# Kernel tuning notes

Hardware: AMD Instinct MI355X
Metric: run time of the kernel (lower is better)

Reference implementation:

```python
import jax, jax.numpy as jnp
import numpy as np

B, S, R, D_NODE, D_PAIR, N_HEAD, C = 1, 128, 256, 256, 128, 8, 32
EPS = 1e-5


def layer_norm(x, g, b):
    mu = jnp.mean(x, axis=-1, keepdims=True)
    var = jnp.mean(jnp.square(x - mu), axis=-1, keepdims=True)
    return (x - mu) * jax.lax.rsqrt(var + EPS) * g + b


def self_attention(x, qkv_w, qkv_b, gate_w, gate_b, o_w, o_b, bias=None):
    # x: [B, n1, n2, d]; attends over n2. heads: n_head x c, n_head*c == d.
    b_, n1, n2, d = x.shape
    qkv = x @ qkv_w.T + qkv_b                      # [B, n1, n2, 3*h*c]
    q, k, v = jnp.split(qkv, 3, axis=-1)
    split_heads = lambda t: t.reshape(b_, n1, n2, N_HEAD, C).transpose(0, 1, 3, 2, 4)  # [B,n1,h,n2,c]
    q = split_heads(q) * (C ** -0.5)
    k = split_heads(k)
    v = split_heads(v)
    logits = jnp.einsum('bshqc,bshkc->bshqk', q, k)  # [B, n1, h, n2, n2]
    if bias is not None:
        logits = logits + bias[:, None]              # bias: [B, h, n2, n2]
    w = jax.nn.softmax(logits, axis=-1)
    o = jnp.einsum('bshqk,bshkc->bshqc', w, v)
    o = o.transpose(0, 1, 3, 2, 4).reshape(b_, n1, n2, N_HEAD * C)
    gate = jax.nn.sigmoid(x @ gate_w.T + gate_b)
    o = o * gate
    out = o @ o_w.T
    if o_b is not None:
        out = out + o_b
    return out


def setup_inputs() -> dict:
    key = jax.random.key(0)
    ks = jax.random.split(key, 12)
    rn = lambda k, sh, sc=1.0: jax.random.normal(k, sh, dtype=jnp.float32) * sc
    return {
        'node': rn(ks[0], (B, S, R, D_NODE)),
        'pair': rn(ks[1], (B, R, R, D_PAIR)),
        'ln_mr_g': jnp.ones((D_NODE,), jnp.float32), 'ln_mr_b': jnp.zeros((D_NODE,), jnp.float32),
        'ln_z_g': jnp.ones((D_PAIR,), jnp.float32), 'ln_z_b': jnp.zeros((D_PAIR,), jnp.float32),
        'b_weights': rn(ks[2], (N_HEAD, D_PAIR), D_PAIR ** -0.5),
        'row_qkv_w': rn(ks[3], (3 * N_HEAD * C, D_NODE), D_NODE ** -0.5),
        'row_qkv_b': jnp.zeros((3 * N_HEAD * C,), jnp.float32),
        'row_gate_w': rn(ks[4], (N_HEAD * C, D_NODE), D_NODE ** -0.5),
        'row_gate_b': jnp.ones((N_HEAD * C,), jnp.float32),
        'row_o_w': rn(ks[5], (D_NODE, N_HEAD * C), D_NODE ** -0.5),
        'out_bias': jnp.zeros((D_NODE,), jnp.float32),
        'ln_mc_g': jnp.ones((D_NODE,), jnp.float32), 'ln_mc_b': jnp.zeros((D_NODE,), jnp.float32),
        'col_qkv_w': rn(ks[6], (3 * N_HEAD * C, D_NODE), D_NODE ** -0.5),
        'col_qkv_b': jnp.zeros((3 * N_HEAD * C,), jnp.float32),
        'col_gate_w': rn(ks[7], (N_HEAD * C, D_NODE), D_NODE ** -0.5),
        'col_gate_b': jnp.ones((N_HEAD * C,), jnp.float32),
        'col_o_w': rn(ks[8], (D_NODE, N_HEAD * C), D_NODE ** -0.5),
        'col_o_b': jnp.zeros((D_NODE,), jnp.float32),
        'ln_t_g': jnp.ones((D_NODE,), jnp.float32), 'ln_t_b': jnp.zeros((D_NODE,), jnp.float32),
        't_w1': rn(ks[9], (4 * D_NODE, D_NODE), D_NODE ** -0.5),
        't_b1': jnp.zeros((4 * D_NODE,), jnp.float32),
        't_w2': rn(ks[10], (D_NODE, 4 * D_NODE), (4 * D_NODE) ** -0.5),
        't_b2': jnp.zeros((D_NODE,), jnp.float32),
    }


def reference(node, pair, ln_mr_g, ln_mr_b, ln_z_g, ln_z_b, b_weights,
              row_qkv_w, row_qkv_b, row_gate_w, row_gate_b, row_o_w, out_bias,
              ln_mc_g, ln_mc_b, col_qkv_w, col_qkv_b, col_gate_w, col_gate_b, col_o_w, col_o_b,
              ln_t_g, ln_t_b, t_w1, t_b1, t_w2, t_b2):
    # --- MSARowAttentionWithPairBias ---
    M = layer_norm(node, ln_mr_g, ln_mr_b)                 # [B,S,R,D]
    Z = layer_norm(pair, ln_z_g, ln_z_b)                   # [B,R,R,Dp]
    b = jnp.einsum('bqkd,hd->bhqk', Z, b_weights)          # pair bias [B,h,R,R]
    M = self_attention(M, row_qkv_w, row_qkv_b, row_gate_w, row_gate_b, row_o_w, None, bias=b)
    # bias_dropout_add with ones dropout mask (inference): residual + (x + bias)
    node = node + M + out_bias
    # --- MSAColumnAttention ---
    Mt = node.transpose(0, 2, 1, 3)                        # [B,R,S,D], attend over S
    Mt = layer_norm(Mt, ln_mc_g, ln_mc_b)
    Mt = self_attention(Mt, col_qkv_w, col_qkv_b, col_gate_w, col_gate_b, col_o_w, col_o_b)
    node = node + Mt.transpose(0, 2, 1, 3)
    # --- MSATransition (n=4) ---
    x = layer_norm(node, ln_t_g, ln_t_b)
    x = jax.nn.relu(x @ t_w1.T + t_b1) @ t_w2.T + t_b2
    return node + x
```

## Files before the change

kernel.cpp:

```cpp
#include <hip/hip_runtime.h>
#include <hip/hip_bf16.h>

#define EPS 1e-5f

typedef __hip_bfloat16 bf16;
typedef __attribute__((ext_vector_type(8))) short short8v;
typedef __attribute__((ext_vector_type(4))) short short4v;
typedef __attribute__((ext_vector_type(4))) float f32x4;

__device__ inline f32x4 mfma16bf(short4v a, short4v b, f32x4 c) {
#if __has_builtin(__builtin_amdgcn_mfma_f32_16x16x16bf16_1k)
  return __builtin_amdgcn_mfma_f32_16x16x16bf16_1k(a, b, c, 0, 0, 0);
#else
  short8v a8 = {a[0], a[1], a[2], a[3], 0, 0, 0, 0};
  short8v b8 = {b[0], b[1], b[2], b[3], 0, 0, 0, 0};
  return __builtin_amdgcn_mfma_f32_16x16x32_bf16(a8, b8, c, 0, 0, 0);
#endif
}

__device__ inline void load_lds16(const void* g, void* l) {
  __builtin_amdgcn_global_load_lds(
      (const __attribute__((address_space(1))) void*)g,
      (__attribute__((address_space(3))) void*)l, 16, 0, 0);
}

__device__ inline unsigned pack_bf16x2(float a, float b) {
  union { bf16 h[2]; unsigned u; } cv;
  cv.h[0] = __float2bfloat16(a);
  cv.h[1] = __float2bfloat16(b);
  return cv.u;
}

__global__ __launch_bounds__(256) void cvt_bf16_kernel(
    const float* __restrict__ in, bf16* __restrict__ out, int n4) {
  int i = blockIdx.x * 256 + threadIdx.x;
  if (i >= n4) return;
  float4 v = reinterpret_cast<const float4*>(in)[i];
  union { ushort4 u; bf16 h[4]; } cv;
  cv.h[0] = __float2bfloat16(v.x);
  cv.h[1] = __float2bfloat16(v.y);
  cv.h[2] = __float2bfloat16(v.z);
  cv.h[3] = __float2bfloat16(v.w);
  reinterpret_cast<ushort4*>(out)[i] = cv.u;
}

__global__ __launch_bounds__(64) void ln256_bf_kernel(
    const float* __restrict__ in, bf16* __restrict__ out,
    const float* __restrict__ g, const float* __restrict__ b) {
  int row = blockIdx.x;
  int lane = threadIdx.x;
  float4 x = reinterpret_cast<const float4*>(in + (size_t)row * 256)[lane];
  float s = x.x + x.y + x.z + x.w;
  float sq = x.x * x.x + x.y * x.y + x.z * x.z + x.w * x.w;
#pragma unroll
  for (int off = 32; off >= 1; off >>= 1) {
    s += __shfl_xor(s, off);
    sq += __shfl_xor(sq, off);
  }
  float mean = s * (1.0f / 256.0f);
  float inv = rsqrtf(sq * (1.0f / 256.0f) - mean * mean + EPS);
  float4 gv = reinterpret_cast<const float4*>(g)[lane];
  float4 bv = reinterpret_cast<const float4*>(b)[lane];
  union { ushort4 u; bf16 h[4]; } cv;
  cv.h[0] = __float2bfloat16((x.x - mean) * inv * gv.x + bv.x);
  cv.h[1] = __float2bfloat16((x.y - mean) * inv * gv.y + bv.y);
  cv.h[2] = __float2bfloat16((x.z - mean) * inv * gv.z + bv.z);
  cv.h[3] = __float2bfloat16((x.w - mean) * inv * gv.w + bv.w);
  reinterpret_cast<ushort4*>(out + (size_t)row * 256)[lane] = cv.u;
}

__global__ __launch_bounds__(64) void pair_bias_kernel(
    const float* __restrict__ pair, const float* __restrict__ g,
    const float* __restrict__ b, const float* __restrict__ bw,
    bf16* __restrict__ bT) {
  int idx = blockIdx.x;
  int q = idx >> 8;
  int k = idx & 255;
  int lane = threadIdx.x;
  float2 z = reinterpret_cast<const float2*>(pair + (size_t)idx * 128)[lane];
  float s = z.x + z.y;
  float sq = z.x * z.x + z.y * z.y;
#pragma unroll
  for (int off = 32; off >= 1; off >>= 1) {
    s += __shfl_xor(s, off);
    sq += __shfl_xor(sq, off);
  }
  float mean = s * (1.0f / 128.0f);
  float inv = rsqrtf(sq * (1.0f / 128.0f) - mean * mean + EPS);
  float2 gv = reinterpret_cast<const float2*>(g)[lane];
  float2 bv = reinterpret_cast<const float2*>(b)[lane];
  float z0 = (z.x - mean) * inv * gv.x + bv.x;
  float z1 = (z.y - mean) * inv * gv.y + bv.y;
#pragma unroll
  for (int h = 0; h < 8; ++h) {
    float2 w = reinterpret_cast<const float2*>(bw + h * 128)[lane];
    float p = z0 * w.x + z1 * w.y;
#pragma unroll
    for (int off = 32; off >= 1; off >>= 1) p += __shfl_xor(p, off);
    if (lane == 0) bT[((size_t)h * 256 + q) * 256 + k] = __float2bfloat16(p);
  }
}

template <int EPI, int AMAP, int OMAP>
__global__ __launch_bounds__(256) void gemm_mfma_kernel(
    const bf16* __restrict__ A, const bf16* __restrict__ W,
    const float* __restrict__ bias, const float* __restrict__ aux, void* out,
    int N, int K, int nbn) {
  __shared__ __align__(16) short As[2][128 * 32];
  __shared__ __align__(16) short Bs[2][128 * 32];
  int nwg = gridDim.x;
  int qch = nwg >> 3;
  int flat = blockIdx.x;
  int wg = (flat & 7) * qch + (flat >> 3);
  int bm = wg / nbn, bn = wg % nbn;
  int tid = threadIdx.x;
  int w = tid >> 6, lane = tid & 63;
  int wr = w >> 1, wc = w & 1;
  int c0 = w * 64 + lane;
  int srow = c0 >> 2, skq = c0 & 3;
  const short* Aptr = (const short*)A;
  const short* Wbase = (const short*)(W + (size_t)(bn * 128) * K);
  f32x4 acc[4][4] = {};
  int lrow = lane & 15, kq = lane >> 4;

  auto arow = [&](int r) -> size_t {
    return AMAP ? ((size_t)r * 256 + bm) : ((size_t)(bm * 128 + r));
  };
  auto stage = [&](int buf, int k0) {
    load_lds16(Aptr + arow(srow) * K + k0 + skq * 8, &As[buf][c0 * 8]);
    load_lds16(Aptr + arow(srow + 64) * K + k0 + skq * 8,
               &As[buf][(256 + c0) * 8]);
    load_lds16(Wbase + (size_t)srow * K + k0 + skq * 8, &Bs[buf][c0 * 8]);
    load_lds16(Wbase + (size_t)(srow + 64) * K + k0 + skq * 8,
               &Bs[buf][(256 + c0) * 8]);
  };

  stage(0, 0);
  __syncthreads();
  int nk = K >> 5;
  for (int t = 0; t < nk; ++t) {
    int cur = t & 1;
    if (t + 1 < nk) stage(cur ^ 1, (t + 1) << 5);
    short8v af[4], bfv[4];
#pragma unroll
    for (int i = 0; i < 4; ++i)
      af[i] = *reinterpret_cast<const short8v*>(
          &As[cur][(wr * 64 + i * 16 + lrow) * 32 + kq * 8]);
#pragma unroll
    for (int j = 0; j < 4; ++j)
      bfv[j] = *reinterpret_cast<const short8v*>(
          &Bs[cur][(wc * 64 + j * 16 + lrow) * 32 + kq * 8]);
#pragma unroll
    for (int i = 0; i < 4; ++i)
#pragma unroll
      for (int j = 0; j < 4; ++j)
        acc[i][j] = __builtin_amdgcn_mfma_f32_16x16x32_bf16(af[i], bfv[j],
                                                            acc[i][j], 0, 0, 0);
    __syncthreads();
  }

  float* outF = (float*)out;
  bf16* outB = (bf16*)out;
  int r4 = (lane >> 4) * 4;
#pragma unroll
  for (int j = 0; j < 4; ++j) {
    int c = bn * 128 + wc * 64 + j * 16 + lrow;
    float bv = bias ? bias[c] : 0.0f;
#pragma unroll
    for (int i = 0; i < 4; ++i) {
      int lr0 = wr * 64 + i * 16 + r4;
#pragma unroll
      for (int reg = 0; reg < 4; ++reg) {
        int lr = lr0 + reg;
        size_t off = OMAP ? (((size_t)lr * 256 + bm) * N + c)
                          : ((size_t)(bm * 128 + lr) * N + c);
        float v = acc[i][j][reg] + bv;
        if (EPI == 0) {
          outB[off] = __float2bfloat16(v);
        } else if (EPI == 2) {
          outF[off] = v + aux[off];
        } else {
          outB[off] = __float2bfloat16(fmaxf(v, 0.0f));
        }
      }
    }
  }
}

template <bool ROWMODE>
__global__ __launch_bounds__(512) void attn_mfma_kernel(
    const bf16* __restrict__ qkv, const bf16* __restrict__ bT,
    bf16* __restrict__ o) {
  constexpr int KVLEN = ROWMODE ? 256 : 128;
  constexpr int QT = ROWMODE ? 2 : 1;
  constexpr int KOUT = KVLEN / 64;
  constexpr int STRIDE = 1024;
  constexpr int NT = 512;
  __shared__ __align__(16) short K_lds[KVLEN * 32];
  __shared__ __align__(16) short Vt_lds[32 * KVLEN];

  int b = blockIdx.x;
  int idx = b >> 3, h = b & 7;
  const short* qb = (const short*)qkv + (size_t)idx * (KVLEN * 1024);
  const bf16* qbh = (const bf16*)qb;
  bf16* ob = o + (size_t)idx * (KVLEN * 256);
  int tid = threadIdx.x;
  int w = tid >> 6, lane = tid & 63;
  int l15 = lane & 15, l4 = lane >> 4;

#pragma unroll
  for (int rnd = 0; rnd < (KVLEN * 4) / NT; ++rnd) {
    int c = rnd * NT + tid;
    int row = c >> 2;
    int kq = (c & 3) ^ ((row >> 1) & 3);
    load_lds16(qb + (size_t)row * STRIDE + 256 + h * 32 + kq * 8,
               &K_lds[c * 8]);
  }
  {
    int tt = tid;
    if (KVLEN * 2 == NT || tt < KVLEN * 2) {
      int kp = tt >> 2;
      int cc = (tt & 3) * 8;
      short8v va = *reinterpret_cast<const short8v*>(
          qb + (size_t)(2 * kp) * STRIDE + 512 + h * 32 + cc);
      short8v vb = *reinterpret_cast<const short8v*>(
          qb + (size_t)(2 * kp + 1) * STRIDE + 512 + h * 32 + cc);
      int k = 2 * kp;
      int u = k >> 3;
      int klo = k & 7;
#pragma unroll
      for (int e = 0; e < 8; ++e) {
        int cI = cc + e;
        int up = u ^ (cI & 7);
        unsigned pk = (unsigned)(unsigned short)va[e] |
                      ((unsigned)(unsigned short)vb[e] << 16);
        *reinterpret_cast<unsigned*>(&Vt_lds[cI * KVLEN + up * 8 + klo]) = pk;
      }
    }
  }
  __syncthreads();

  int q0 = w * QT * 16;
  short8v qf[QT];
#pragma unroll
  for (int j = 0; j < QT; ++j)
    qf[j] = *reinterpret_cast<const short8v*>(
        qb + (size_t)(q0 + j * 16 + l15) * STRIDE + h * 32 + l4 * 8);

  float lrun[QT];
#pragma unroll
  for (int j = 0; j < QT; ++j) lrun[j] = 0.0f;
  f32x4 acc_o[QT][2] = {};

  const float SC = 0.17677669529663687f;
  const float L2E = 1.4426950408889634f;
  const f32x4 zf = {0.f, 0.f, 0.f, 0.f};

#pragma unroll 1
  for (int kt = 0; kt < KOUT; ++kt) {
    ushort4 bb[QT][4];
    if (ROWMODE) {
#pragma unroll
      for (int j = 0; j < QT; ++j) {
        const bf16* bq = bT + (size_t)h * 65536 +
                         (size_t)(q0 + j * 16 + l15) * 256 + kt * 64 + l4 * 4;
#pragma unroll
        for (int i = 0; i < 4; ++i)
          bb[j][i] = *reinterpret_cast<const ushort4*>(bq + i * 16);
      }
    }
    short8v kf[4];
#pragma unroll
    for (int i = 0; i < 4; ++i) {
      int krow = kt * 64 + i * 16 + l15;
      kf[i] = *reinterpret_cast<const short8v*>(
          &K_lds[krow * 32 + ((l4 ^ ((krow >> 1) & 3)) * 8)]);
    }
    short4v vfa[4][2];
#pragma unroll
    for (int ks4 = 0; ks4 < 4; ++ks4)
#pragma unroll
      for (int ct = 0; ct < 2; ++ct) {
        int cI = ct * 16 + l15;
        int u = kt * 8 + ks4 * 2 + (l4 >> 1);
        vfa[ks4][ct] = *reinterpret_cast<const short4v*>(
            &Vt_lds[cI * KVLEN + (u ^ (cI & 7)) * 8 + (l4 & 1) * 4]);
      }

#pragma unroll
    for (int j = 0; j < QT; ++j) {
      f32x4 accs[4];
#pragma unroll
      for (int i = 0; i < 4; ++i)
        accs[i] =
            __builtin_amdgcn_mfma_f32_16x16x32_bf16(kf[i], qf[j], zf, 0, 0, 0);
      float sum = 0.0f;
#pragma unroll
      for (int i = 0; i < 4; ++i) {
        if (ROWMODE) {
          union { ushort4 u; bf16 h4[4]; } bu;
          bu.u = bb[j][i];
#pragma unroll
          for (int r = 0; r < 4; ++r)
            accs[i][r] = accs[i][r] * SC + __bfloat162float(bu.h4[r]);
        } else {
#pragma unroll
          for (int r = 0; r < 4; ++r) accs[i][r] *= SC;
        }
#pragma unroll
        for (int r = 0; r < 4; ++r) {
          float p = exp2f(accs[i][r] * L2E);
          accs[i][r] = p;
          sum += p;
        }
      }
      sum += __shfl_xor(sum, 16);
      sum += __shfl_xor(sum, 32);
      lrun[j] += sum;
#pragma unroll
      for (int ks4 = 0; ks4 < 4; ++ks4) {
        union { unsigned u2[2]; short4v s; } pb;
        pb.u2[0] = pack_bf16x2(accs[ks4][0], accs[ks4][1]);
        pb.u2[1] = pack_bf16x2(accs[ks4][2], accs[ks4][3]);
#pragma unroll
        for (int ct = 0; ct < 2; ++ct)
          acc_o[j][ct] = mfma16bf(vfa[ks4][ct], pb.s, acc_o[j][ct]);
      }
    }
  }

#pragma unroll
  for (int j = 0; j < QT; ++j) {
    float inv = 1.0f / lrun[j];
    int row = q0 + j * 16 + l15;
    const bf16* grow = qbh + (size_t)row * STRIDE + 768 + h * 32;
    bf16* orow = ob + (size_t)row * 256 + h * 32;
#pragma unroll
    for (int ct = 0; ct < 2; ++ct) {
      int cc = ct * 16 + l4 * 4;
      ushort4 gv = *reinterpret_cast<const ushort4*>(grow + cc);
      union { ushort4 u; bf16 h4[4]; } gu, ou;
      gu.u = gv;
#pragma unroll
      for (int r = 0; r < 4; ++r) {
        float gt = __bfloat162float(gu.h4[r]);
        float sg = 1.0f / (1.0f + __expf(-gt));
        ou.h4[r] = __float2bfloat16(acc_o[j][ct][r] * inv * sg);
      }
      *reinterpret_cast<ushort4*>(orow + cc) = ou.u;
    }
  }
}

extern "C" void kernel_launch(void* const* d_in, const int* in_sizes, int n_in,
                              void* d_out, int out_size, void* d_ws,
                              size_t ws_size, hipStream_t stream) {
  (void)in_sizes; (void)n_in; (void)out_size; (void)ws_size;
  const float* node      = (const float*)d_in[0];
  const float* pair      = (const float*)d_in[1];
  const float* ln_mr_g   = (const float*)d_in[2];
  const float* ln_mr_b   = (const float*)d_in[3];
  const float* ln_z_g    = (const float*)d_in[4];
  const float* ln_z_b    = (const float*)d_in[5];
  const float* b_weights = (const float*)d_in[6];
  const float* row_qkv_w = (const float*)d_in[7];
  const float* row_qkv_b = (const float*)d_in[8];
  const float* row_gate_w= (const float*)d_in[9];
  const float* row_gate_b= (const float*)d_in[10];
  const float* row_o_w   = (const float*)d_in[11];
  const float* out_bias  = (const float*)d_in[12];
  const float* ln_mc_g   = (const float*)d_in[13];
  const float* ln_mc_b   = (const float*)d_in[14];
  const float* col_qkv_w = (const float*)d_in[15];
  const float* col_qkv_b = (const float*)d_in[16];
  const float* col_gate_w= (const float*)d_in[17];
  const float* col_gate_b= (const float*)d_in[18];
  const float* col_o_w   = (const float*)d_in[19];
  const float* col_o_b   = (const float*)d_in[20];
  const float* ln_t_g    = (const float*)d_in[21];
  const float* ln_t_b    = (const float*)d_in[22];
  const float* t_w1      = (const float*)d_in[23];
  const float* t_b1      = (const float*)d_in[24];
  const float* t_w2      = (const float*)d_in[25];
  const float* t_b2      = (const float*)d_in[26];
  float* out = (float*)d_out;

  const size_t NR = 32768;
  char* p = (char*)d_ws;
  float* buf_node = (float*)p; p += NR * 256 * 4;
  char*  qkv_region = p;       p += NR * 1024 * 2;
  bf16* buf_bias  = (bf16*)p;  p += 8 * 256 * 256 * 2;
  bf16* ln_bf     = (bf16*)p;  p += NR * 256 * 2;
  bf16* g_bf      = (bf16*)p;  p += NR * 256 * 2;
  bf16* qkv_bf = (bf16*)qkv_region;
  bf16* h_bf   = (bf16*)qkv_region;
  bf16* w_rqkvg = (bf16*)p; p += 1024 * 256 * 2;
  bf16* w_ro    = (bf16*)p; p += 256 * 256 * 2;
  bf16* w_cqkvg = (bf16*)p; p += 1024 * 256 * 2;
  bf16* w_co    = (bf16*)p; p += 256 * 256 * 2;
  bf16* w_t1    = (bf16*)p; p += 1024 * 256 * 2;
  bf16* w_t2    = (bf16*)p; p += 256 * 1024 * 2;
  float* b_rqkvg = (float*)p; p += 1024 * 4;
  float* b_cqkvg = (float*)p; p += 1024 * 4;

  cvt_bf16_kernel<<<192, 256, 0, stream>>>(row_qkv_w, w_rqkvg, 49152);
  cvt_bf16_kernel<<<64, 256, 0, stream>>>(row_gate_w, w_rqkvg + 768 * 256,
                                          16384);
  cvt_bf16_kernel<<<64, 256, 0, stream>>>(row_o_w, w_ro, 16384);
  cvt_bf16_kernel<<<192, 256, 0, stream>>>(col_qkv_w, w_cqkvg, 49152);
  cvt_bf16_kernel<<<64, 256, 0, stream>>>(col_gate_w, w_cqkvg + 768 * 256,
                                          16384);
  cvt_bf16_kernel<<<64, 256, 0, stream>>>(col_o_w, w_co, 16384);
  cvt_bf16_kernel<<<256, 256, 0, stream>>>(t_w1, w_t1, 65536);
  cvt_bf16_kernel<<<256, 256, 0, stream>>>(t_w2, w_t2, 65536);
  hipMemcpyAsync(b_rqkvg, row_qkv_b, 768 * 4, hipMemcpyDeviceToDevice, stream);
  hipMemcpyAsync(b_rqkvg + 768, row_gate_b, 256 * 4, hipMemcpyDeviceToDevice,
                 stream);
  hipMemcpyAsync(b_cqkvg, col_qkv_b, 768 * 4, hipMemcpyDeviceToDevice, stream);
  hipMemcpyAsync(b_cqkvg + 768, col_gate_b, 256 * 4, hipMemcpyDeviceToDevice,
                 stream);

  ln256_bf_kernel<<<32768, 64, 0, stream>>>(node, ln_bf, ln_mr_g, ln_mr_b);
  pair_bias_kernel<<<65536, 64, 0, stream>>>(pair, ln_z_g, ln_z_b, b_weights,
                                             buf_bias);
  gemm_mfma_kernel<0, 0, 0><<<2048, 256, 0, stream>>>(
      ln_bf, w_rqkvg, b_rqkvg, nullptr, qkv_bf, 1024, 256, 8);
  attn_mfma_kernel<true><<<1024, 512, 0, stream>>>(qkv_bf, buf_bias, g_bf);
  gemm_mfma_kernel<2, 0, 0><<<512, 256, 0, stream>>>(
      g_bf, w_ro, out_bias, node, buf_node, 256, 256, 2);

  ln256_bf_kernel<<<32768, 64, 0, stream>>>(buf_node, ln_bf, ln_mc_g, ln_mc_b);
  gemm_mfma_kernel<0, 1, 0><<<2048, 256, 0, stream>>>(
      ln_bf, w_cqkvg, b_cqkvg, nullptr, qkv_bf, 1024, 256, 8);
  attn_mfma_kernel<false><<<2048, 512, 0, stream>>>(qkv_bf, nullptr, g_bf);
  gemm_mfma_kernel<2, 0, 1><<<512, 256, 0, stream>>>(
      g_bf, w_co, col_o_b, buf_node, buf_node, 256, 256, 2);

  ln256_bf_kernel<<<32768, 64, 0, stream>>>(buf_node, ln_bf, ln_t_g, ln_t_b);
  gemm_mfma_kernel<3, 0, 0><<<2048, 256, 0, stream>>>(
      ln_bf, w_t1, t_b1, nullptr, h_bf, 1024, 256, 8);
  gemm_mfma_kernel<2, 0, 0><<<512, 256, 0, stream>>>(
      h_bf, w_t2, t_b2, buf_node, out, 256, 1024, 2);
}
```

Before: 358.0 us.

## Compute pair bias projection with MFMA over 16-row tiles per wave

Rewrites the pair bias kernel so that each wave layer-norms 16 pair rows and projects them onto the 8 head weights with a bf16 16x16x32 MFMA. This replaces one 64-thread block per row, which used eight serial shuffle reductions. The grid shrinks from 65536 tiny blocks to 1024 blocks of 256 threads, cutting launch and reduction overhead. The bias is now computed from bf16-rounded normalized activations and weights rather than in fp32, and half of the MFMA columns are padding.

Result: faster. 325.5 us (-9.1%).

```diff
diff --git a/kernel.cpp b/kernel.cpp
--- a/kernel.cpp
+++ b/kernel.cpp
@@ -69,35 +69,72 @@
   reinterpret_cast<ushort4*>(out + (size_t)row * 256)[lane] = cv.u;
 }
 
-__global__ __launch_bounds__(64) void pair_bias_kernel(
+__global__ __launch_bounds__(256) void pair_bias_kernel(
     const float* __restrict__ pair, const float* __restrict__ g,
     const float* __restrict__ b, const float* __restrict__ bw,
     bf16* __restrict__ bT) {
-  int idx = blockIdx.x;
-  int q = idx >> 8;
-  int k = idx & 255;
-  int lane = threadIdx.x;
-  float2 z = reinterpret_cast<const float2*>(pair + (size_t)idx * 128)[lane];
-  float s = z.x + z.y;
-  float sq = z.x * z.x + z.y * z.y;
-#pragma unroll
-  for (int off = 32; off >= 1; off >>= 1) {
-    s += __shfl_xor(s, off);
-    sq += __shfl_xor(sq, off);
-  }
-  float mean = s * (1.0f / 128.0f);
-  float inv = rsqrtf(sq * (1.0f / 128.0f) - mean * mean + EPS);
-  float2 gv = reinterpret_cast<const float2*>(g)[lane];
-  float2 bv = reinterpret_cast<const float2*>(b)[lane];
-  float z0 = (z.x - mean) * inv * gv.x + bv.x;
-  float z1 = (z.y - mean) * inv * gv.y + bv.y;
-#pragma unroll
-  for (int h = 0; h < 8; ++h) {
-    float2 w = reinterpret_cast<const float2*>(bw + h * 128)[lane];
-    float p = z0 * w.x + z1 * w.y;
-#pragma unroll
-    for (int off = 32; off >= 1; off >>= 1) p += __shfl_xor(p, off);
-    if (lane == 0) bT[((size_t)h * 256 + q) * 256 + k] = __float2bfloat16(p);
+  int tid = threadIdx.x;
+  int w = tid >> 6, lane = tid & 63;
+  int l15 = lane & 15, l4 = lane >> 4;
+  int rowbase = blockIdx.x * 64 + w * 16;
+  const float* zrow = pair + (size_t)(rowbase + l15) * 128;
+
+  float z[4][8];
+#pragma unroll
+  for (int kk = 0; kk < 4; ++kk) {
+    float4 a0 = *reinterpret_cast<const float4*>(zrow + kk * 32 + l4 * 8);
+    float4 a1 = *reinterpret_cast<const float4*>(zrow + kk * 32 + l4 * 8 + 4);
+    z[kk][0] = a0.x; z[kk][1] = a0.y; z[kk][2] = a0.z; z[kk][3] = a0.w;
+    z[kk][4] = a1.x; z[kk][5] = a1.y; z[kk][6] = a1.z; z[kk][7] = a1.w;
+  }
+  float s = 0.0f, sq = 0.0f;
+#pragma unroll
+  for (int kk = 0; kk < 4; ++kk)
+#pragma unroll
+    for (int e = 0; e < 8; ++e) {
+      s += z[kk][e];
+      sq += z[kk][e] * z[kk][e];
+    }
+  s += __shfl_xor(s, 16);
+  s += __shfl_xor(s, 32);
+  sq += __shfl_xor(sq, 16);
+  sq += __shfl_xor(sq, 32);
+  float mu = s * (1.0f / 128.0f);
+  float inv = rsqrtf(sq * (1.0f / 128.0f) - mu * mu + EPS);
+
+  f32x4 acc = {0.f, 0.f, 0.f, 0.f};
+#pragma unroll
+  for (int kk = 0; kk < 4; ++kk) {
+    const float* gp = g + kk * 32 + l4 * 8;
+    const float* bp = b + kk * 32 + l4 * 8;
+    float4 g0 = *reinterpret_cast<const float4*>(gp);
+    float4 g1 = *reinterpret_cast<const float4*>(gp + 4);
+    float4 b0 = *reinterpret_cast<const float4*>(bp);
+    float4 b1 = *reinterpret_cast<const float4*>(bp + 4);
+    float gv[8] = {g0.x, g0.y, g0.z, g0.w, g1.x, g1.y, g1.z, g1.w};
+    float bv[8] = {b0.x, b0.y, b0.z, b0.w, b1.x, b1.y, b1.z, b1.w};
+    union { short8v v; bf16 h[8]; } af;
+#pragma unroll
+    for (int e = 0; e < 8; ++e)
+      af.h[e] = __float2bfloat16((z[kk][e] - mu) * inv * gv[e] + bv[e]);
+    union { short8v v; bf16 h[8]; } bwf;
+    if (l15 < 8) {
+      const float* wp = bw + l15 * 128 + kk * 32 + l4 * 8;
+      float4 w0 = *reinterpret_cast<const float4*>(wp);
+      float4 w1 = *reinterpret_cast<const float4*>(wp + 4);
+      float wv[8] = {w0.x, w0.y, w0.z, w0.w, w1.x, w1.y, w1.z, w1.w};
+#pragma unroll
+      for (int e = 0; e < 8; ++e) bwf.h[e] = __float2bfloat16(wv[e]);
+    } else {
+      bwf.v = short8v{0, 0, 0, 0, 0, 0, 0, 0};
+    }
+    acc = __builtin_amdgcn_mfma_f32_16x16x32_bf16(af.v, bwf.v, acc, 0, 0, 0);
+  }
+  if (l15 < 8) {
+#pragma unroll
+    for (int r = 0; r < 4; ++r)
+      bT[(size_t)l15 * 65536 + rowbase + l4 * 4 + r] =
+          __float2bfloat16(acc[r]);
   }
 }
 
@@ -421,7 +458,7 @@
                  stream);
 
   ln256_bf_kernel<<<32768, 64, 0, stream>>>(node, ln_bf, ln_mr_g, ln_mr_b);
-  pair_bias_kernel<<<65536, 64, 0, stream>>>(pair, ln_z_g, ln_z_b, b_weights,
+  pair_bias_kernel<<<1024, 256, 0, stream>>>(pair, ln_z_g, ln_z_b, b_weights,
                                              buf_bias);
   gemm_mfma_kernel<0, 0, 0><<<2048, 256, 0, stream>>>(
       ln_bf, w_rqkvg, b_rqkvg, nullptr, qkv_bf, 1024, 256, 8);
```
